# Performance work log

Measured on AMD Instinct MI355X. Metric: run time of the kernel, lower is better.

The kernel has to match this reference:

```python
import jax, jax.numpy as jnp
import numpy as np

B, C, H, W = 32, 1536, 32, 32
M_CLUSTERS, L_DIM, G_DIM = 64, 128, 256
SINKHORN_ITERS = 3
EPS = 1e-12

def setup_inputs() -> dict:
    key = jax.random.key(0)
    ks = jax.random.split(key, 16)
    s = lambda i, shape, scale=0.02: jax.random.normal(ks[i], shape, jnp.float32) * scale
    return {
        'x': jax.random.normal(ks[0], (B, C, H, W), jnp.float32),
        't': jax.random.normal(ks[1], (B, C), jnp.float32),
        'cf_w1': s(2, (512, C)), 'cf_b1': s(3, (512,)),
        'cf_w2': s(4, (L_DIM, 512)), 'cf_b2': s(5, (L_DIM,)),
        'sc_w1': s(6, (512, C)), 'sc_b1': s(7, (512,)),
        'sc_w2': s(8, (M_CLUSTERS, 512)), 'sc_b2': s(9, (M_CLUSTERS,)),
        'tk_w1': s(10, (512, C)), 'tk_b1': s(11, (512,)),
        'tk_w2': s(12, (G_DIM, 512)), 'tk_b2': s(13, (G_DIM,)),
        'dust_bin': jnp.array(1.0, jnp.float32),
    }

def _l2norm(v, axis):
    n = jnp.sqrt(jnp.sum(v * v, axis=axis, keepdims=True))
    return v / jnp.maximum(n, EPS)

def _log_optimal_transport(scores, alpha, iters):
    # scores: [B, m, n]; append dustbin row, run log-space Sinkhorn
    b, m, n = scores.shape
    norm = -jnp.log(jnp.float32(m + n))
    bins = jnp.broadcast_to(alpha, (b, 1, n))
    Z0 = jnp.concatenate([scores, bins], axis=1)             # [B, m+1, n]
    log_mu = jnp.concatenate([jnp.full((m,), norm, jnp.float32),
                              jnp.log(jnp.float32(n - m))[None] + norm])  # [m+1]
    log_nu = jnp.full((n,), norm, jnp.float32)               # [n]
    u = jnp.zeros((b, m + 1), jnp.float32)
    v = jnp.zeros((b, n), jnp.float32)
    for _ in range(iters):
        u = log_mu[None, :] - jax.nn.logsumexp(Z0 + v[:, None, :], axis=2)
        v = log_nu[None, :] - jax.nn.logsumexp(Z0 + u[:, :, None], axis=1)
    return Z0 + u[:, :, None] + v[:, None, :] - norm

def reference(x, t, cf_w1, cf_b1, cf_w2, cf_b2, sc_w1, sc_b1, sc_w2, sc_b2,
              tk_w1, tk_b1, tk_w2, tk_b2, dust_bin):
    b = x.shape[0]
    xf = x.reshape(b, x.shape[1], -1)                        # [B, C, HW]
    # cluster_features: 1x1 conv stack -> [B, l, HW]
    h = jax.nn.relu(jnp.einsum('oc,bcn->bon', cf_w1, xf) + cf_b1[None, :, None])
    f = jnp.einsum('oc,bcn->bon', cf_w2, h) + cf_b2[None, :, None]
    # score: 1x1 conv stack -> [B, m, HW]
    h = jax.nn.relu(jnp.einsum('oc,bcn->bon', sc_w1, xf) + sc_b1[None, :, None])
    p = jnp.einsum('oc,bcn->bon', sc_w2, h) + sc_b2[None, :, None]
    # token_features: MLP -> [B, g]
    tk = jax.nn.relu(t @ tk_w1.T + tk_b1) @ tk_w2.T + tk_b2
    # Sinkhorn OT assignment, drop dustbin row
    p = jnp.exp(_log_optimal_transport(p, dust_bin, SINKHORN_ITERS))[:, :-1, :]  # [B, m, HW]
    # fused VLAD aggregation (avoids the repeat-materialized tensors)
    agg = jnp.einsum('bln,bmn->blm', f, p)                   # [B, l, m]
    agg = _l2norm(agg, axis=1).reshape(b, -1)                # [B, l*m]
    v = jnp.concatenate([_l2norm(tk, axis=-1), agg], axis=-1)
    return _l2norm(v, axis=-1)
```

## Files before the change

kernel.cpp:

```cpp
#include <hip/hip_runtime.h>
#include <hip/hip_bf16.h>
#include <math.h>

typedef unsigned short u16;
typedef __attribute__((ext_vector_type(8))) short short8;
typedef __attribute__((ext_vector_type(4))) float floatx4;

#define DEVINL __device__ __forceinline__

DEVINL float bf2f(u16 u) { union { unsigned int i; float f; } v; v.i = ((unsigned int)u) << 16; return v.f; }
DEVINL u16 f2bf(float f) {
  union { unsigned int i; float f; } v; v.f = f;
  unsigned int i = v.i;
  unsigned int r = (i + 0x7fffu + ((i >> 16) & 1u)) >> 16;
  return (u16)r;
}

__global__ __launch_bounds__(256) void k_prep(
    const float* __restrict__ cf_w1, u16* __restrict__ wc1,
    const float* __restrict__ sc_w1, u16* __restrict__ ws1,
    const float* __restrict__ cf_w2, u16* __restrict__ wc2,
    const float* __restrict__ sc_w2, u16* __restrict__ ws2p,
    const float* __restrict__ sc_b2, float* __restrict__ scb2p) {
  int i = blockIdx.x * 256 + threadIdx.x;
  int job = blockIdx.y;
  if (job == 4) {
    if (i < 128) scb2p[i] = (i < 64) ? sc_b2[i] : 0.f;
    return;
  }
  const float* src = (job == 0) ? cf_w1 : (job == 1) ? sc_w1 : (job == 2) ? cf_w2 : sc_w2;
  u16* dst = (job == 0) ? wc1 : (job == 1) ? ws1 : (job == 2) ? wc2 : ws2p;
  int n4 = (job <= 1) ? 196608 : 16384;
  if (i >= n4) return;
  ushort4 o = {0, 0, 0, 0};
  if (job != 3 || (i >> 7) < 64) {
    float4 v = ((const float4*)src)[i];
    o.x = f2bf(v.x); o.y = f2bf(v.y); o.z = f2bf(v.z); o.w = f2bf(v.w);
  }
  ((ushort4*)dst)[i] = o;
}

__global__ __launch_bounds__(256) void k_transpose(const float* __restrict__ x,
                                                   u16* __restrict__ xT,
                                                   int nC, int nN) {
  __shared__ u16 tile[64 * 65];
  int b = blockIdx.z;
  int c0 = blockIdx.y * 64, n0 = blockIdx.x * 64;
  const float* xb = x + ((long)b * nC + c0) * nN + n0;
  u16* xTb = xT + ((long)b * nN + n0) * nC + c0;
  int tid = threadIdx.x;
#pragma unroll
  for (int p = 0; p < 2; ++p) {
    int u = tid + p * 256;
    int r = u >> 3, nc = (u & 7) * 8;
    const float4* srcp = (const float4*)(xb + (long)r * nN + nc);
    float4 v0 = srcp[0], v1 = srcp[1];
    int base = r * 65 + nc;
    tile[base + 0] = f2bf(v0.x); tile[base + 1] = f2bf(v0.y);
    tile[base + 2] = f2bf(v0.z); tile[base + 3] = f2bf(v0.w);
    tile[base + 4] = f2bf(v1.x); tile[base + 5] = f2bf(v1.y);
    tile[base + 6] = f2bf(v1.z); tile[base + 7] = f2bf(v1.w);
  }
  __syncthreads();
#pragma unroll
  for (int p = 0; p < 2; ++p) {
    int u = tid + p * 256;
    int nr = u >> 3, cc = (u & 7) * 8;
    __align__(16) u16 tmp[8];
#pragma unroll
    for (int j = 0; j < 8; ++j) tmp[j] = tile[(cc + j) * 65 + nr];
    *(uint4*)(xTb + (long)nr * nC + cc) = *(uint4*)(tmp);
  }
}

template <bool OUT_F32, int BIAS_MODE, bool RELU>
__global__ __launch_bounds__(256) void k_gemm64(
    const u16* __restrict__ A, int lda, long aBS,
    const u16* __restrict__ B1, const u16* __restrict__ B2, int nSplit,
    int ldb, long bBS,
    void* __restrict__ Out, int ldo, long oBS,
    const float* __restrict__ bias1, const float* __restrict__ bias2,
    int M, int N, int K) {
  __shared__ __align__(16) u16 As[128 * 64];
  __shared__ __align__(16) u16 Bs[128 * 64];
  int bz = blockIdx.z;
  int m0 = blockIdx.x * 128, n0 = blockIdx.y * 128;
  const u16* Ablk = A + (long)bz * aBS + (long)m0 * lda;
  const u16* Bblk =
      ((n0 < nSplit) ? (B1 + (long)n0 * ldb) : (B2 + (long)(n0 - nSplit) * ldb)) +
      (long)bz * bBS;
  int tid = threadIdx.x;
  int lane = tid & 63;
  int lane16 = lane & 15, quad = lane >> 4;
  int wid = tid >> 6;
  int wm = wid >> 1, wn = wid & 1;

  int rIn = lane >> 3;
  int kkSw = ((lane & 7) ^ rIn) * 8;

  floatx4 acc[4][4];
#pragma unroll
  for (int i = 0; i < 4; ++i)
#pragma unroll
    for (int j = 0; j < 4; ++j) acc[i][j] = (floatx4){0.f, 0.f, 0.f, 0.f};

  for (int k0 = 0; k0 < K; k0 += 64) {
    __syncthreads();
#pragma unroll
    for (int h = 0; h < 4; ++h) {
      int ch = wid * 4 + h;
      int r = ch * 8 + rIn;
      const u16* srcA = Ablk + (long)r * lda + k0 + kkSw;
      __builtin_amdgcn_global_load_lds(
          (const __attribute__((address_space(1))) void*)srcA,
          (__attribute__((address_space(3))) void*)&As[ch * 512], 16, 0, 0);
      const u16* srcB = Bblk + (long)r * ldb + k0 + kkSw;
      __builtin_amdgcn_global_load_lds(
          (const __attribute__((address_space(1))) void*)srcB,
          (__attribute__((address_space(3))) void*)&Bs[ch * 512], 16, 0, 0);
    }
    __syncthreads();
#pragma unroll
    for (int h2 = 0; h2 < 2; ++h2) {
      short8 af[4], bfr[4];
#pragma unroll
      for (int t = 0; t < 4; ++t) {
        int ra = wm * 64 + t * 16 + lane16;
        af[t] = *(const short8*)&As[ra * 64 + (((h2 * 4 + quad) ^ (ra & 7)) * 8)];
      }
#pragma unroll
      for (int t = 0; t < 4; ++t) {
        int rb = wn * 64 + t * 16 + lane16;
        bfr[t] = *(const short8*)&Bs[rb * 64 + (((h2 * 4 + quad) ^ (rb & 7)) * 8)];
      }
#pragma unroll
      for (int i = 0; i < 4; ++i)
#pragma unroll
        for (int j = 0; j < 4; ++j)
          acc[i][j] = __builtin_amdgcn_mfma_f32_16x16x32_bf16(af[i], bfr[j],
                                                              acc[i][j], 0, 0, 0);
    }
  }

  const float* bcolPtr = bias1;
  int bofs = 0;
  if (BIAS_MODE == 2 && n0 >= nSplit) { bcolPtr = bias2; bofs = nSplit; }
#pragma unroll
  for (int i = 0; i < 4; ++i) {
    int rowb = m0 + wm * 64 + i * 16 + quad * 4;
#pragma unroll
    for (int j = 0; j < 4; ++j) {
      int col = n0 + wn * 64 + j * 16 + lane16;
      float bc = 0.f;
      if (BIAS_MODE == 2) bc = bcolPtr[col - bofs];
#pragma unroll
      for (int r = 0; r < 4; ++r) {
        int row = rowb + r;
        float v = acc[i][j][r];
        if (BIAS_MODE == 2) v += bc;
        if (BIAS_MODE == 1) v += bias1[row];
        if (RELU) v = fmaxf(v, 0.f);
        if (OUT_F32)
          ((float*)Out)[(long)bz * oBS + (long)row * ldo + col] = v;
        else
          ((u16*)Out)[(long)bz * oBS + (long)row * ldo + col] = f2bf(v);
      }
    }
  }
}

__global__ __launch_bounds__(256) void k_k2dual(
    const u16* __restrict__ wA, const u16* __restrict__ wB,
    const u16* __restrict__ hT, u16* __restrict__ fOut, u16* __restrict__ sOut,
    const float* __restrict__ bA, const float* __restrict__ bB) {
  __shared__ __align__(16) u16 As[128 * 64];
  __shared__ __align__(16) u16 Bs[128 * 64];
  int sel = blockIdx.y, bz = blockIdx.z;
  const u16* A = sel ? wB : wA;
  const u16* Bbase = hT + (long)bz * 1048576 + (sel ? 512 : 0);
  u16* Out = (sel ? sOut : fOut) + (long)bz * 131072;
  const float* bias = sel ? bB : bA;
  int n0 = blockIdx.x * 128;
  int tid = threadIdx.x;
  int lane = tid & 63;
  int lane16 = lane & 15, quad = lane >> 4;
  int wid = tid >> 6;
  int wm = wid >> 1, wn = wid & 1;
  int rIn = lane >> 3;
  int kkSw = ((lane & 7) ^ rIn) * 8;

  floatx4 acc[4][4];
#pragma unroll
  for (int i = 0; i < 4; ++i)
#pragma unroll
    for (int j = 0; j < 4; ++j) acc[i][j] = (floatx4){0.f, 0.f, 0.f, 0.f};

  for (int k0 = 0; k0 < 512; k0 += 64) {
    __syncthreads();
#pragma unroll
    for (int h = 0; h < 4; ++h) {
      int ch = wid * 4 + h;
      int r = ch * 8 + rIn;
      const u16* srcA = A + (long)r * 512 + k0 + kkSw;
      __builtin_amdgcn_global_load_lds(
          (const __attribute__((address_space(1))) void*)srcA,
          (__attribute__((address_space(3))) void*)&As[ch * 512], 16, 0, 0);
      const u16* srcB = Bbase + (long)(n0 + r) * 1024 + k0 + kkSw;
      __builtin_amdgcn_global_load_lds(
          (const __attribute__((address_space(1))) void*)srcB,
          (__attribute__((address_space(3))) void*)&Bs[ch * 512], 16, 0, 0);
    }
    __syncthreads();
#pragma unroll
    for (int h2 = 0; h2 < 2; ++h2) {
      short8 af[4], bfr[4];
#pragma unroll
      for (int t = 0; t < 4; ++t) {
        int ra = wm * 64 + t * 16 + lane16;
        af[t] = *(const short8*)&As[ra * 64 + (((h2 * 4 + quad) ^ (ra & 7)) * 8)];
      }
#pragma unroll
      for (int t = 0; t < 4; ++t) {
        int rb = wn * 64 + t * 16 + lane16;
        bfr[t] = *(const short8*)&Bs[rb * 64 + (((h2 * 4 + quad) ^ (rb & 7)) * 8)];
      }
#pragma unroll
      for (int i = 0; i < 4; ++i)
#pragma unroll
        for (int j = 0; j < 4; ++j)
          acc[i][j] = __builtin_amdgcn_mfma_f32_16x16x32_bf16(af[i], bfr[j],
                                                              acc[i][j], 0, 0, 0);
    }
  }
#pragma unroll
  for (int i = 0; i < 4; ++i) {
    int rowb = wm * 64 + i * 16 + quad * 4;
#pragma unroll
    for (int j = 0; j < 4; ++j) {
      int col = n0 + wn * 64 + j * 16 + lane16;
#pragma unroll
      for (int r = 0; r < 4; ++r) {
        int row = rowb + r;
        Out[(long)row * 1024 + col] = f2bf(acc[i][j][r] + bias[row]);
      }
    }
  }
}

__global__ __launch_bounds__(1024) void k_sinkhorn(
    const u16* __restrict__ S, const float* __restrict__ alphaPtr,
    float lmu, float lmu_bin, float lnu, float norm, u16* __restrict__ P) {
  __shared__ float u_[65];
  __shared__ float v_[1024];
  int b = blockIdx.x, tid = threadIdx.x;
  const u16* Sb = S + (long)b * 131072;
  float alpha = *alphaPtr;
  v_[tid] = 0.f;
  __syncthreads();
  int wid = tid >> 6, lane = tid & 63;
  for (int it = 0; it < 3; ++it) {
    for (int i = wid; i < 65; i += 16) {
      float vals[16];
      float mx = -3.4e38f;
#pragma unroll
      for (int s = 0; s < 16; ++s) {
        int j = lane + s * 64;
        float z = (i < 64 ? bf2f(Sb[i * 1024 + j]) : alpha) + v_[j];
        vals[s] = z;
        mx = fmaxf(mx, z);
      }
#pragma unroll
      for (int off = 32; off > 0; off >>= 1) mx = fmaxf(mx, __shfl_xor(mx, off));
      float sum = 0.f;
#pragma unroll
      for (int s = 0; s < 16; ++s) sum += __expf(vals[s] - mx);
#pragma unroll
      for (int off = 32; off > 0; off >>= 1) sum += __shfl_xor(sum, off);
      if (lane == 0) u_[i] = (i < 64 ? lmu : lmu_bin) - (mx + __logf(sum));
    }
    __syncthreads();
    {
      float mx = alpha + u_[64];
#pragma unroll 8
      for (int i = 0; i < 64; ++i)
        mx = fmaxf(mx, bf2f(Sb[i * 1024 + tid]) + u_[i]);
      float sum = __expf(alpha + u_[64] - mx);
#pragma unroll 8
      for (int i = 0; i < 64; ++i)
        sum += __expf(bf2f(Sb[i * 1024 + tid]) + u_[i] - mx);
      v_[tid] = lnu - (mx + __logf(sum));
    }
    __syncthreads();
  }
  float vj = v_[tid];
  u16* Pb = P + (long)b * 65536;
#pragma unroll 8
  for (int i = 0; i < 64; ++i) {
    float z = bf2f(Sb[i * 1024 + tid]) + u_[i] + vj - norm;
    Pb[i * 1024 + tid] = f2bf(__expf(fminf(z, 1.0f)));
  }
}

__global__ __launch_bounds__(256) void k_agg(const u16* __restrict__ f,
                                             const u16* __restrict__ P,
                                             float* __restrict__ aggP) {
  __shared__ __align__(16) u16 Fs[128 * 32];
  __shared__ __align__(16) u16 Ps[64 * 32];
  int bz = blockIdx.z, kc = blockIdx.x;
  const u16* Fb = f + (long)bz * 128 * 1024;
  const u16* Pb = P + (long)bz * 64 * 1024;
  int tid = threadIdx.x, wid = tid >> 6, lane = tid & 63;
  int lane16 = lane & 15, quad = lane >> 4;
  int rA0 = lane >> 2, kk = (lane & 3) * 8;

  floatx4 acc[2][4];
#pragma unroll
  for (int i = 0; i < 2; ++i)
#pragma unroll
    for (int j = 0; j < 4; ++j) acc[i][j] = (floatx4){0.f, 0.f, 0.f, 0.f};

  for (int k0 = kc * 256; k0 < kc * 256 + 256; k0 += 32) {
    __syncthreads();
#pragma unroll
    for (int h = 0; h < 2; ++h) {
      int ch = wid * 2 + h;
      int r = ch * 16 + rA0;
      const u16* srcF = Fb + (long)r * 1024 + k0 + kk;
      __builtin_amdgcn_global_load_lds(
          (const __attribute__((address_space(1))) void*)srcF,
          (__attribute__((address_space(3))) void*)&Fs[ch * 512], 16, 0, 0);
    }
    {
      int r = wid * 16 + rA0;
      const u16* srcP = Pb + (long)r * 1024 + k0 + kk;
      __builtin_amdgcn_global_load_lds(
          (const __attribute__((address_space(1))) void*)srcP,
          (__attribute__((address_space(3))) void*)&Ps[wid * 512], 16, 0, 0);
    }
    __syncthreads();
    short8 af[2], bfr[4];
#pragma unroll
    for (int t = 0; t < 2; ++t)
      af[t] = *(const short8*)&Fs[(wid * 32 + t * 16 + lane16) * 32 + quad * 8];
#pragma unroll
    for (int j = 0; j < 4; ++j)
      bfr[j] = *(const short8*)&Ps[(j * 16 + lane16) * 32 + quad * 8];
#pragma unroll
    for (int i = 0; i < 2; ++i)
#pragma unroll
      for (int j = 0; j < 4; ++j)
        acc[i][j] = __builtin_amdgcn_mfma_f32_16x16x32_bf16(af[i], bfr[j],
                                                            acc[i][j], 0, 0, 0);
  }
  float* ab = aggP + ((long)kc * 32 + bz) * 8192;
#pragma unroll
  for (int i = 0; i < 2; ++i)
#pragma unroll
    for (int j = 0; j < 4; ++j)
#pragma unroll
      for (int r = 0; r < 4; ++r) {
        int row = wid * 32 + i * 16 + quad * 4 + r;
        int col = j * 16 + lane16;
        ab[row * 64 + col] = acc[i][j][r];
      }
}

DEVINL float waveSum(float x) {
#pragma unroll
  for (int off = 32; off > 0; off >>= 1) x += __shfl_xor(x, off);
  return x;
}

__global__ __launch_bounds__(256) void k_mlp1(const float* __restrict__ t,
                                              const float* __restrict__ w1,
                                              const float* __restrict__ b1,
                                              float* __restrict__ h1) {
  __shared__ float tl[1536];
  int b = blockIdx.y, og = blockIdx.x;
  int tid = threadIdx.x, wid = tid >> 6, lane = tid & 63;
  for (int i = tid; i < 1536; i += 256) tl[i] = t[b * 1536 + i];
  __syncthreads();
#pragma unroll 4
  for (int oi = 0; oi < 16; ++oi) {
    int o = og * 64 + wid * 16 + oi;
    const float* wr = w1 + (long)o * 1536;
    float acc = 0.f;
#pragma unroll
    for (int s = 0; s < 24; ++s) { int c = lane + s * 64; acc += tl[c] * wr[c]; }
    acc = waveSum(acc);
    if (lane == 0) h1[b * 512 + o] = fmaxf(acc + b1[o], 0.f);
  }
}

__global__ __launch_bounds__(256) void k_mlp2(const float* __restrict__ h1,
                                              const float* __restrict__ w2,
                                              const float* __restrict__ b2,
                                              float* __restrict__ tk) {
  __shared__ float hl[512];
  int b = blockIdx.y, og = blockIdx.x;
  int tid = threadIdx.x, wid = tid >> 6, lane = tid & 63;
  for (int i = tid; i < 512; i += 256) hl[i] = h1[b * 512 + i];
  __syncthreads();
#pragma unroll 4
  for (int oi = 0; oi < 16; ++oi) {
    int o = og * 64 + wid * 16 + oi;
    const float* wr = w2 + (long)o * 512;
    float acc = 0.f;
#pragma unroll
    for (int s = 0; s < 8; ++s) { int c = lane + s * 64; acc += hl[c] * wr[c]; }
    acc = waveSum(acc);
    if (lane == 0) tk[b * 256 + o] = acc + b2[o];
  }
}

DEVINL float blockSum256(float x, float* red) {
#pragma unroll
  for (int off = 32; off > 0; off >>= 1) x += __shfl_xor(x, off);
  int wid = threadIdx.x >> 6;
  __syncthreads();
  if ((threadIdx.x & 63) == 0) red[wid] = x;
  __syncthreads();
  return red[0] + red[1] + red[2] + red[3];
}

__global__ __launch_bounds__(256) void k_norms(const float* __restrict__ tk,
                                               const float* __restrict__ aggP,
                                               float* __restrict__ out) {
  __shared__ float asum[8192];
  __shared__ float cn[64];
  __shared__ float red[4];
  int b = blockIdx.x, tid = threadIdx.x;
  const float* a0 = aggP + (long)b * 8192;
  for (int idx = tid; idx < 8192; idx += 256)
    asum[idx] = a0[idx] + a0[32 * 8192 + idx] + a0[64 * 8192 + idx] +
                a0[96 * 8192 + idx];
  __syncthreads();
  float tkv = tk[b * 256 + tid];
  float tss = blockSum256(tkv * tkv, red);
  float tn = fmaxf(sqrtf(tss), 1e-12f);
  if (tid < 64) {
    float s = 0.f;
    for (int l = 0; l < 128; ++l) { float a = asum[l * 64 + tid]; s += a * a; }
    cn[tid] = fmaxf(sqrtf(s), 1e-12f);
  }
  __syncthreads();
  float gs = (tkv / tn) * (tkv / tn);
  for (int idx = tid; idx < 8192; idx += 256) {
    float a = asum[idx] / cn[idx & 63];
    gs += a * a;
  }
  float G = blockSum256(gs, red);
  float inv = 1.f / fmaxf(sqrtf(G), 1e-12f);
  float* ob = out + (long)b * 8448;
  ob[tid] = tkv / tn * inv;
  for (int idx = tid; idx < 8192; idx += 256)
    ob[256 + idx] = asum[idx] / cn[idx & 63] * inv;
}

extern "C" void kernel_launch(void* const* d_in, const int* in_sizes, int n_in,
                              void* d_out, int out_size, void* d_ws,
                              size_t ws_size, hipStream_t stream) {
  const float* x = (const float*)d_in[0];
  const float* t = (const float*)d_in[1];
  const float* cf_w1 = (const float*)d_in[2];
  const float* cf_b1 = (const float*)d_in[3];
  const float* cf_w2 = (const float*)d_in[4];
  const float* cf_b2 = (const float*)d_in[5];
  const float* sc_w1 = (const float*)d_in[6];
  const float* sc_b1 = (const float*)d_in[7];
  const float* sc_w2 = (const float*)d_in[8];
  const float* sc_b2 = (const float*)d_in[9];
  const float* tk_w1 = (const float*)d_in[10];
  const float* tk_b1 = (const float*)d_in[11];
  const float* tk_w2 = (const float*)d_in[12];
  const float* tk_b2 = (const float*)d_in[13];
  const float* dust = (const float*)d_in[14];
  float* out = (float*)d_out;

  char* ws = (char*)d_ws;
  size_t off = 0;
  u16* wc1 = (u16*)(ws + off); off += (size_t)512 * 1536 * 2;
  u16* ws1 = (u16*)(ws + off); off += (size_t)512 * 1536 * 2;
  u16* wc2 = (u16*)(ws + off); off += (size_t)128 * 512 * 2;
  u16* ws2p = (u16*)(ws + off); off += (size_t)128 * 512 * 2;
  float* scb2p = (float*)(ws + off); off += (size_t)128 * 4;
  u16* f = (u16*)(ws + off);   off += (size_t)32 * 128 * 1024 * 2;
  u16* scr = (u16*)(ws + off); off += (size_t)32 * 128 * 1024 * 2;
  u16* P = (u16*)(ws + off);   off += (size_t)32 * 64 * 1024 * 2;
  float* aggP = (float*)(ws + off); off += (size_t)4 * 32 * 128 * 64 * 4;
  float* h1ws = (float*)(ws + off); off += (size_t)32 * 512 * 4;
  float* tkws = (float*)(ws + off); off += (size_t)32 * 256 * 4;
  size_t fixed = off;
  size_t perB = (size_t)1024 * 1536 * 2 + (size_t)1024 * 1024 * 2;
  int c = 1;
  const int cands[6] = {32, 16, 8, 4, 2, 1};
  for (int k = 0; k < 6; ++k)
    if (fixed + (size_t)cands[k] * perB <= ws_size) { c = cands[k]; break; }
  u16* xT = (u16*)(ws + fixed);
  u16* hT = (u16*)(ws + fixed + (size_t)c * 1024 * 1536 * 2);

  k_prep<<<dim3(768, 5), 256, 0, stream>>>(cf_w1, wc1, sc_w1, ws1, cf_w2, wc2,
                                           sc_w2, ws2p, sc_b2, scb2p);

  k_mlp1<<<dim3(8, 32), 256, 0, stream>>>(t, tk_w1, tk_b1, h1ws);
  k_mlp2<<<dim3(4, 32), 256, 0, stream>>>(h1ws, tk_w2, tk_b2, tkws);

  float norm = -logf(1088.f);
  float lmu = norm;
  float lmu_bin = logf(960.f) + norm;
  float lnu = norm;

  for (int cb = 0; cb < 32; cb += c) {
    k_transpose<<<dim3(16, 24, c), 256, 0, stream>>>(
        x + (size_t)cb * 1536 * 1024, xT, 1536, 1024);
    k_gemm64<false, 2, true><<<dim3(8, 8, c), 256, 0, stream>>>(
        xT, 1536, (long)1024 * 1536,
        wc1, ws1, 512, 1536, 0,
        hT, 1024, (long)1024 * 1024,
        cf_b1, sc_b1, 1024, 1024, 1536);
    k_k2dual<<<dim3(8, 2, c), 256, 0, stream>>>(
        wc2, ws2p, hT, f + (size_t)cb * 131072, scr + (size_t)cb * 131072,
        cf_b2, scb2p);
  }
  k_sinkhorn<<<32, 1024, 0, stream>>>(scr, dust, lmu, lmu_bin, lnu, norm, P);
  k_agg<<<dim3(4, 1, 32), 256, 0, stream>>>(f, P, aggP);
  k_norms<<<32, 256, 0, stream>>>(tkws, aggP, out);
}
```

Baseline: 599.0 us.

## Replace first-layer GEMM with 256x256 tiled, double-buffered pipelined MFMA kernel

The generic 128x128 GEMM for the first 1x1 conv layer is replaced by a specialized 256x256-tile kernel with 8 waves. It double-buffers the LDS tiles and interleaves async global-to-LDS loads with MFMA phases, using explicit waitcnt, barriers and setprio. The aim is to hide load latency and raise data reuse per tile. In exchange it uses more LDS and registers per block and launches fewer blocks, and it hardcodes the problem dimensions.

```diff
diff --git a/kernel.cpp b/kernel.cpp
--- a/kernel.cpp
+++ b/kernel.cpp
@@ -73,97 +73,127 @@
   }
 }
 
-template <bool OUT_F32, int BIAS_MODE, bool RELU>
-__global__ __launch_bounds__(256) void k_gemm64(
-    const u16* __restrict__ A, int lda, long aBS,
-    const u16* __restrict__ B1, const u16* __restrict__ B2, int nSplit,
-    int ldb, long bBS,
-    void* __restrict__ Out, int ldo, long oBS,
-    const float* __restrict__ bias1, const float* __restrict__ bias2,
-    int M, int N, int K) {
-  __shared__ __align__(16) u16 As[128 * 64];
-  __shared__ __align__(16) u16 Bs[128 * 64];
+
+#define K1_STAGE(S, H, SB)                                                     \
+  if ((S) <= 23) {                                                             \
+    const u16* gb_ = ((H) < 2) ? Bb : Ab;                                      \
+    u16* lb_ = ((H) < 2) ? &Bs[SB][(H) & 1][0] : &As[SB][(H) & 1][0];          \
+    int k0_ = (S) << 6;                                                        \
+    _Pragma("unroll") for (int l_ = 0; l_ < 2; ++l_) {                         \
+      int r_ = (wid * 2 + l_) * 8 + rIn;                                       \
+      const u16* src_ =                                                        \
+          gb_ + (long)(((H) & 1) * 128 + r_) * 1536 + k0_ + cSw;               \
+      __builtin_amdgcn_global_load_lds(                                        \
+          (const __attribute__((address_space(1))) void*)src_,                 \
+          (__attribute__((address_space(3))) void*)(lb_ + (wid * 2 + l_) * 512), \
+          16, 0, 0);                                                           \
+    }                                                                          \
+  }
+
+#define K1_PHASE(P, SS, SH, SB, VMN)                                           \
+  {                                                                            \
+    short8 a00 = *(const short8*)(Aw + ((P)*2 + 0) * 1024 + aB0);              \
+    short8 a01 = *(const short8*)(Aw + ((P)*2 + 0) * 1024 + aB1);              \
+    short8 a10 = *(const short8*)(Aw + ((P)*2 + 1) * 1024 + aB0);              \
+    short8 a11 = *(const short8*)(Aw + ((P)*2 + 1) * 1024 + aB1);              \
+    if ((P) == 0) {                                                            \
+      _Pragma("unroll") for (int n2 = 0; n2 < 4; ++n2) {                       \
+        b[n2][0] = *(const short8*)(Bw + n2 * 1024 + aB0);                     \
+        b[n2][1] = *(const short8*)(Bw + n2 * 1024 + aB1);                     \
+      }                                                                        \
+    }                                                                          \
+    K1_STAGE(SS, SH, SB)                                                       \
+    __builtin_amdgcn_s_barrier();                                              \
+    asm volatile("s_waitcnt lgkmcnt(0)" ::: "memory");                         \
+    __builtin_amdgcn_s_setprio(1);                                             \
+    _Pragma("unroll") for (int n2 = 0; n2 < 4; ++n2) {                         \
+      acc[(P)*2][n2] = __builtin_amdgcn_mfma_f32_16x16x32_bf16(                \
+          a00, b[n2][0], acc[(P)*2][n2], 0, 0, 0);                             \
+      acc[(P)*2][n2] = __builtin_amdgcn_mfma_f32_16x16x32_bf16(                \
+          a01, b[n2][1], acc[(P)*2][n2], 0, 0, 0);                             \
+      acc[(P)*2 + 1][n2] = __builtin_amdgcn_mfma_f32_16x16x32_bf16(            \
+          a10, b[n2][0], acc[(P)*2 + 1][n2], 0, 0, 0);                         \
+      acc[(P)*2 + 1][n2] = __builtin_amdgcn_mfma_f32_16x16x32_bf16(            \
+          a11, b[n2][1], acc[(P)*2 + 1][n2], 0, 0, 0);                         \
+    }                                                                          \
+    __builtin_amdgcn_s_setprio(0);                                             \
+    if ((VMN) == 6) {                                                          \
+      asm volatile("s_waitcnt vmcnt(6)" ::: "memory");                         \
+    } else if ((VMN) == 0) {                                                   \
+      asm volatile("s_waitcnt vmcnt(0)" ::: "memory");                         \
+    }                                                                          \
+    __builtin_amdgcn_s_barrier();                                              \
+  }
+
+#define K1_TILE(T, BUF, VM)                                                    \
+  {                                                                            \
+    const u16* Aw = &As[BUF][wm][0];                                           \
+    const u16* Bw = &Bs[BUF][wn >> 1][(wn & 1) * 4096];                        \
+    short8 b[4][2];                                                            \
+    K1_PHASE(0, (T) + 1, 3, (BUF) ^ 1, -1)                                     \
+    K1_PHASE(1, (T) + 2, 0, (BUF), -1)                                         \
+    K1_PHASE(2, (T) + 2, 1, (BUF), -1)                                         \
+    K1_PHASE(3, (T) + 2, 2, (BUF), (VM))                                       \
+  }
+
+__global__ __launch_bounds__(512, 2) void k_gemm256(
+    const u16* __restrict__ A,
+    const u16* __restrict__ B1, const u16* __restrict__ B2,
+    u16* __restrict__ Out,
+    const float* __restrict__ bias1, const float* __restrict__ bias2) {
+  __shared__ __align__(16) u16 As[2][2][8192];
+  __shared__ __align__(16) u16 Bs[2][2][8192];
   int bz = blockIdx.z;
-  int m0 = blockIdx.x * 128, n0 = blockIdx.y * 128;
-  const u16* Ablk = A + (long)bz * aBS + (long)m0 * lda;
-  const u16* Bblk =
-      ((n0 < nSplit) ? (B1 + (long)n0 * ldb) : (B2 + (long)(n0 - nSplit) * ldb)) +
-      (long)bz * bBS;
+  int m0 = blockIdx.x * 256, n0 = blockIdx.y * 256;
+  const u16* Ab = A + ((long)bz * 1024 + m0) * 1536;
+  const u16* Bb = (n0 < 512) ? (B1 + (long)n0 * 1536)
+                             : (B2 + (long)(n0 - 512) * 1536);
   int tid = threadIdx.x;
   int lane = tid & 63;
+  int wid = tid >> 6;
+  int wm = wid >> 2, wn = wid & 3;
   int lane16 = lane & 15, quad = lane >> 4;
-  int wid = tid >> 6;
-  int wm = wid >> 1, wn = wid & 1;
-
   int rIn = lane >> 3;
-  int kkSw = ((lane & 7) ^ rIn) * 8;
-
-  floatx4 acc[4][4];
-#pragma unroll
-  for (int i = 0; i < 4; ++i)
+  int cSw = ((lane & 7) ^ rIn) << 3;
+  int aB0 = lane16 * 64 + ((quad ^ (lane16 & 7)) << 3);
+  int aB1 = lane16 * 64 + (((4 + quad) ^ (lane16 & 7)) << 3);
+
+  floatx4 acc[8][4];
+#pragma unroll
+  for (int i = 0; i < 8; ++i)
 #pragma unroll
     for (int j = 0; j < 4; ++j) acc[i][j] = (floatx4){0.f, 0.f, 0.f, 0.f};
 
-  for (int k0 = 0; k0 < K; k0 += 64) {
-    __syncthreads();
-#pragma unroll
-    for (int h = 0; h < 4; ++h) {
-      int ch = wid * 4 + h;
-      int r = ch * 8 + rIn;
-      const u16* srcA = Ablk + (long)r * lda + k0 + kkSw;
-      __builtin_amdgcn_global_load_lds(
-          (const __attribute__((address_space(1))) void*)srcA,
-          (__attribute__((address_space(3))) void*)&As[ch * 512], 16, 0, 0);
-      const u16* srcB = Bblk + (long)r * ldb + k0 + kkSw;
-      __builtin_amdgcn_global_load_lds(
-          (const __attribute__((address_space(1))) void*)srcB,
-          (__attribute__((address_space(3))) void*)&Bs[ch * 512], 16, 0, 0);
-    }
-    __syncthreads();
-#pragma unroll
-    for (int h2 = 0; h2 < 2; ++h2) {
-      short8 af[4], bfr[4];
-#pragma unroll
-      for (int t = 0; t < 4; ++t) {
-        int ra = wm * 64 + t * 16 + lane16;
-        af[t] = *(const short8*)&As[ra * 64 + (((h2 * 4 + quad) ^ (ra & 7)) * 8)];
-      }
-#pragma unroll
-      for (int t = 0; t < 4; ++t) {
-        int rb = wn * 64 + t * 16 + lane16;
-        bfr[t] = *(const short8*)&Bs[rb * 64 + (((h2 * 4 + quad) ^ (rb & 7)) * 8)];
-      }
-#pragma unroll
-      for (int i = 0; i < 4; ++i)
-#pragma unroll
-        for (int j = 0; j < 4; ++j)
-          acc[i][j] = __builtin_amdgcn_mfma_f32_16x16x32_bf16(af[i], bfr[j],
-                                                              acc[i][j], 0, 0, 0);
-    }
-  }
-
-  const float* bcolPtr = bias1;
-  int bofs = 0;
-  if (BIAS_MODE == 2 && n0 >= nSplit) { bcolPtr = bias2; bofs = nSplit; }
-#pragma unroll
-  for (int i = 0; i < 4; ++i) {
-    int rowb = m0 + wm * 64 + i * 16 + quad * 4;
-#pragma unroll
-    for (int j = 0; j < 4; ++j) {
-      int col = n0 + wn * 64 + j * 16 + lane16;
-      float bc = 0.f;
-      if (BIAS_MODE == 2) bc = bcolPtr[col - bofs];
+  K1_STAGE(0, 0, 0)
+  K1_STAGE(0, 1, 0)
+  K1_STAGE(0, 2, 0)
+  K1_STAGE(0, 3, 0)
+  K1_STAGE(1, 0, 1)
+  K1_STAGE(1, 1, 1)
+  K1_STAGE(1, 2, 1)
+  asm volatile("s_waitcnt vmcnt(6)" ::: "memory");
+  __builtin_amdgcn_s_barrier();
+
+  for (int it = 0; it < 11; ++it) {
+    K1_TILE(2 * it, 0, 6)
+    K1_TILE(2 * it + 1, 1, 6)
+  }
+  K1_TILE(22, 0, 0)
+  K1_TILE(23, 1, -1)
+
+  const float* bcol = (n0 < 512) ? (bias1 + n0) : (bias2 + (n0 - 512));
+  long obase = (long)bz * 1048576;
+#pragma unroll
+  for (int mi = 0; mi < 8; ++mi) {
+    int row0 = m0 + wm * 128 + mi * 16 + quad * 4;
+#pragma unroll
+    for (int ni = 0; ni < 4; ++ni) {
+      int colw = wn * 64 + ni * 16 + lane16;
+      float bb = bcol[colw];
 #pragma unroll
       for (int r = 0; r < 4; ++r) {
-        int row = rowb + r;
-        float v = acc[i][j][r];
-        if (BIAS_MODE == 2) v += bc;
-        if (BIAS_MODE == 1) v += bias1[row];
-        if (RELU) v = fmaxf(v, 0.f);
-        if (OUT_F32)
-          ((float*)Out)[(long)bz * oBS + (long)row * ldo + col] = v;
-        else
-          ((u16*)Out)[(long)bz * oBS + (long)row * ldo + col] = f2bf(v);
+        float v = fmaxf(acc[mi][ni][r] + bb, 0.f);
+        Out[obase + (long)(row0 + r) * 1024 + n0 + colw] = f2bf(v);
       }
     }
   }
@@ -513,11 +543,8 @@
   for (int cb = 0; cb < 32; cb += c) {
     k_transpose<<<dim3(16, 24, c), 256, 0, stream>>>(
         x + (size_t)cb * 1536 * 1024, xT, 1536, 1024);
-    k_gemm64<false, 2, true><<<dim3(8, 8, c), 256, 0, stream>>>(
-        xT, 1536, (long)1024 * 1536,
-        wc1, ws1, 512, 1536, 0,
-        hT, 1024, (long)1024 * 1024,
-        cf_b1, sc_b1, 1024, 1024, 1536);
+    k_gemm256<<<dim3(4, 4, c), 512, 0, stream>>>(xT, wc1, ws1, hT, cf_b1,
+                                                 sc_b1);
     k_k2dual<<<dim3(8, 2, c), 256, 0, stream>>>(
         wc2, ws2p, hT, f + (size_t)cb * 131072, scr + (size_t)cb * 131072,
         cf_b2, scb2p);
```

Result: faster. 567.4 us (-5.3%).
